# Kernel tuning notes

Measured on AMD Instinct MI355X. Metric: run time of the kernel, lower is better.

The kernel has to match this reference:

```python
import jax, jax.numpy as jnp
import numpy as np

HEADS = 8
NEG_SLOPE = 0.2


def _layer_norm(x, g, b, eps=1e-5):
    mu = x.mean(-1, keepdims=True)
    var = ((x - mu) ** 2).mean(-1, keepdims=True)
    return (x - mu) / jnp.sqrt(var + eps) * g + b


def setup_inputs() -> dict:
    key = jax.random.key(0)
    ks = jax.random.split(key, 24)
    N, E, H, L = 512, 260000, 256, 4
    s = 0.05
    return dict(
        x=jax.random.normal(ks[0], (N, 1), jnp.float32),
        edge_index=jax.random.randint(ks[1], (2, E), 0, N),
        edge_attr=jax.random.uniform(ks[2], (E, 3), jnp.float32),
        emb_W=jax.random.normal(ks[3], (1, H)) * s,
        emb_b=jnp.zeros((H,)),
        Wl=jax.random.normal(ks[4], (L, H, H)) * s,
        bl=jnp.zeros((L, H)),
        Wr=jax.random.normal(ks[5], (L, H, H)) * s,
        br=jnp.zeros((L, H)),
        We=jax.random.normal(ks[6], (L, 3, H)) * s,
        att=jax.random.normal(ks[7], (L, HEADS, H // HEADS)) * s,
        gb=jnp.zeros((L, H)),
        ln_g=jnp.ones((L, H)),
        ln_b=jnp.zeros((L, H)),
        p1_W=jax.random.normal(ks[8], (2 * H, H)) * s,
        p1_b=jnp.zeros((H,)),
        p2_W=jax.random.normal(ks[9], (H, H // 2)) * s,
        p2_b=jnp.zeros((H // 2,)),
        p3_W=jax.random.normal(ks[10], (H // 2, 1)) * s,
        p3_b=jnp.zeros((1,)),
        v1_W=jax.random.normal(ks[11], (2 * H, H)) * s,
        v1_b=jnp.zeros((H,)),
        v2_W=jax.random.normal(ks[12], (H, 1)) * s,
        v2_b=jnp.zeros((1,)),
        coupling=jnp.asarray(1.0, jnp.float32),
    )


def reference(x, edge_index, edge_attr, emb_W, emb_b, Wl, bl, Wr, br, We, att,
              gb, ln_g, ln_b, p1_W, p1_b, p2_W, p2_b, p3_W, p3_b,
              v1_W, v1_b, v2_W, v2_b, coupling):
    N = x.shape[0]
    E = edge_attr.shape[0]
    L = Wl.shape[0]
    C = Wl.shape[-1] // HEADS
    src, dst = edge_index[0], edge_index[1]

    # PyG GATv2Conv adds self-loops with edge_attr fill_value='mean'
    # (mean of incoming edge_attr per destination node).
    sums = jax.ops.segment_sum(edge_attr, dst, num_segments=N)
    cnt = jax.ops.segment_sum(jnp.ones((E,), edge_attr.dtype), dst, num_segments=N)
    self_attr = sums / jnp.maximum(cnt, 1.0)[:, None]
    loop = jnp.arange(N)
    src_f = jnp.concatenate([src, loop])            # [E+N]
    dst_f = jnp.concatenate([dst, loop])
    ea_f = jnp.concatenate([edge_attr, self_attr])  # [E+N, 3]

    h = x @ emb_W + emb_b                           # [N, H]
    for l in range(L):
        res = h
        xl = (h @ Wl[l] + bl[l]).reshape(N, HEADS, C)
        xr = (h @ Wr[l] + br[l]).reshape(N, HEADS, C)
        ee = (ea_f @ We[l]).reshape(-1, HEADS, C)
        # GATv2 scoring: leaky_relu(x_l[src]+x_r[dst]+edge) . att
        m = jax.nn.leaky_relu(xl[src_f] + xr[dst_f] + ee, NEG_SLOPE)
        alpha = jnp.einsum('ehc,hc->eh', m, att[l])
        amax = jax.ops.segment_max(alpha, dst_f, num_segments=N)
        alpha = jnp.exp(alpha - amax[dst_f])
        denom = jax.ops.segment_sum(alpha, dst_f, num_segments=N)
        alpha = alpha / denom[dst_f]
        out = jax.ops.segment_sum(xl[src_f] * alpha[..., None], dst_f,
                                  num_segments=N).reshape(N, HEADS * C) + gb[l]
        h = jax.nn.relu(_layer_norm(out + res, ln_g[l], ln_b[l]))

    # graph-level representation (single graph, batch=None branch)
    graph_repr = jnp.concatenate([h.mean(0, keepdims=True),
                                  h.max(0, keepdims=True)], axis=1)  # [1, 2H]

    # all-pairs edge representations (i < j)
    iu, ju = jnp.triu_indices(N, k=1)
    er = jnp.concatenate([h[iu], h[ju]], axis=1)    # [N(N-1)/2, 2H]
    p = jax.nn.relu(er @ p1_W + p1_b)
    p = jax.nn.relu(p @ p2_W + p2_b)
    policy_logits = (p @ p3_W + p3_b).squeeze(-1)   # [N(N-1)/2]

    v = jax.nn.relu(graph_repr @ v1_W + v1_b)
    value = (v @ v2_W + v2_b).squeeze(-1)           # [1]

    # Potts energy: per-color degree-squared approximation of triangles
    colors = jnp.argmax(edge_attr, axis=1)
    energy = jnp.asarray(0.0, h.dtype)
    for c in (1, 2):
        w = (colors == c).astype(h.dtype)
        deg = (jax.ops.segment_sum(w, src, num_segments=N)
               + jax.ops.segment_sum(w, dst, num_segments=N))
        energy = energy + (deg ** 2).sum() / (2.0 * N)
    energy = energy * coupling

    return policy_logits, value, energy
```

## Files before the change

### kernel.cpp

```cpp
#include <hip/hip_runtime.h>
#include <math.h>

#define HDIM 256
#define NHEADS 8
#define NEG 0.2f
#define NB 256
#define SEG 4

typedef float f32x4 __attribute__((ext_vector_type(4)));
typedef _Float16 f16x8 __attribute__((ext_vector_type(8)));
typedef __fp16 fp16v2 __attribute__((ext_vector_type(2)));

__global__ __launch_bounds__(256) void edge_part(
    const int* __restrict__ ei, const float* __restrict__ ea, int E, int CH,
    int* __restrict__ pcnt, float* __restrict__ psum, int* __restrict__ pcol) {
  __shared__ int   lcnt[512];
  __shared__ float ls0[512], ls1[512], ls2[512];
  __shared__ int   lcol[1024];
  int t = threadIdx.x, b = blockIdx.x;
  for (int n = t; n < 512; n += 256) {
    lcnt[n] = 0; ls0[n] = 0.f; ls1[n] = 0.f; ls2[n] = 0.f;
    lcol[n] = 0; lcol[512 + n] = 0;
  }
  __syncthreads();
  int e0 = b * CH, e1 = min(E, e0 + CH);
  for (int e = e0 + t; e < e1; e += 256) {
    int src = ei[e], dst = ei[E + e];
    float a0 = ea[3*e], a1 = ea[3*e+1], a2 = ea[3*e+2];
    atomicAdd(&lcnt[dst], 1);
    atomicAdd(&ls0[dst], a0);
    atomicAdd(&ls1[dst], a1);
    atomicAdd(&ls2[dst], a2);
    int idx = 0; float best = a0;
    if (a1 > best) { best = a1; idx = 1; }
    if (a2 > best) { idx = 2; }
    if (idx) {
      int o = (idx - 1) << 9;
      atomicAdd(&lcol[o + src], 1);
      atomicAdd(&lcol[o + dst], 1);
    }
  }
  __syncthreads();
  for (int n = t; n < 512; n += 256) {
    pcnt[b*512 + n] = lcnt[n];
    psum[(size_t)(0*NB + b)*512 + n] = ls0[n];
    psum[(size_t)(1*NB + b)*512 + n] = ls1[n];
    psum[(size_t)(2*NB + b)*512 + n] = ls2[n];
    pcol[(size_t)(0*NB + b)*512 + n] = lcol[n];
    pcol[(size_t)(1*NB + b)*512 + n] = lcol[512 + n];
  }
}

__global__ __launch_bounds__(256) void red_kernel(
    const int* __restrict__ pcnt, const float* __restrict__ psum,
    const int* __restrict__ pcol,
    int* __restrict__ cnt, float* __restrict__ sred, int* __restrict__ dred,
    int* __restrict__ pbase) {
  int q = blockIdx.x >> 1;
  int n = (blockIdx.x & 1)*256 + threadIdx.x;
  if (q == 0) {
    int run = 0;
#pragma unroll 8
    for (int b = 0; b < NB; ++b) {
      int v = pcnt[b*512 + n];
      pbase[b*512 + n] = run;
      run += v;
    }
    cnt[n] = run;
  } else if (q <= 3) {
    int qq = q - 1;
    float s = 0.f;
#pragma unroll 8
    for (int b = 0; b < NB; ++b) s += psum[(size_t)(qq*NB + b)*512 + n];
    sred[qq*512 + n] = s;
  } else {
    int qq = q - 4;
    int s = 0;
#pragma unroll 8
    for (int b = 0; b < NB; ++b) s += pcol[(size_t)(qq*NB + b)*512 + n];
    dred[qq*512 + n] = s;
  }
}

__global__ __launch_bounds__(512) void scan2(
    const int* __restrict__ cnt, const float* __restrict__ sred,
    const int* __restrict__ dred, int N,
    int* __restrict__ rowp, float4* __restrict__ csr,
    const float* __restrict__ coupling, float* __restrict__ eout) {
  int t = threadIdx.x;
  int c = (t < N) ? cnt[t] : 0;
  __shared__ int sbuf[512];
  int v = (t < N) ? (c + 1) : 0;
  sbuf[t] = v;
  __syncthreads();
  for (int off = 1; off < 512; off <<= 1) {
    int add = (t >= off) ? sbuf[t - off] : 0;
    __syncthreads();
    sbuf[t] += add;
    __syncthreads();
  }
  int incl = sbuf[t], excl = incl - v;
  if (t < N) {
    rowp[t] = excl;
    if (t == N - 1) rowp[N] = incl;
    float inv = 1.f / fmaxf((float)c, 1.f);
    csr[excl] = make_float4(sred[t]*inv, sred[512 + t]*inv, sred[1024 + t]*inv,
                            __int_as_float(t));
  }
  float e = 0.f;
  if (t < N) {
    float d1 = (float)dred[t], d2 = (float)dred[512 + t];
    e = d1*d1 + d2*d2;
  }
#pragma unroll
  for (int off = 1; off < 64; off <<= 1) e += __shfl_xor(e, off);
  __shared__ float wred[8];
  if ((t & 63) == 0) wred[t >> 6] = e;
  __syncthreads();
  if (t == 0) {
    float s = 0.f;
#pragma unroll
    for (int i = 0; i < 8; ++i) s += wred[i];
    eout[0] = coupling[0] * s / (2.f * (float)N);
  }
}

__global__ __launch_bounds__(256) void scatter2(
    const int* __restrict__ ei, const float* __restrict__ ea, int E, int CH,
    const int* __restrict__ rowp, const int* __restrict__ pbase,
    float4* __restrict__ csr) {
  __shared__ int lofs[512];
  int t = threadIdx.x, b = blockIdx.x;
  for (int n = t; n < 512; n += 256) lofs[n] = 0;
  __syncthreads();
  int e0 = b * CH, e1 = min(E, e0 + CH);
  for (int e = e0 + t; e < e1; e += 256) {
    int src = ei[e], dst = ei[E + e];
    float a0 = ea[3*e], a1 = ea[3*e+1], a2 = ea[3*e+2];
    int lp = atomicAdd(&lofs[dst], 1);
    int pos = rowp[dst] + 1 + pbase[b*512 + dst] + lp;
    csr[pos] = make_float4(a0, a1, a2, __int_as_float(src));
  }
}

__global__ __launch_bounds__(256) void emb_kernel(
    const float* __restrict__ x, const float* __restrict__ eW,
    const float* __restrict__ eb, float* __restrict__ h) {
  int n = blockIdx.x, t = threadIdx.x;
  h[n*HDIM + t] = fmaf(x[n], eW[t], eb[t]);
}

__global__ __launch_bounds__(256) void w_prep_all(
    const float* __restrict__ Wl, const float* __restrict__ Wr,
    const float* __restrict__ p1W, unsigned short* __restrict__ dst) {
  int gid = blockIdx.x * 256 + threadIdx.x;
  int s = gid >> 16, e = gid & 65535;
  int k = e >> 8, n = e & 255;
  const float* src = (s < 4) ? (Wl + (size_t)s*65536)
                   : (s < 8) ? (Wr + (size_t)(s-4)*65536)
                             : (p1W + (size_t)(s-8)*65536);
  int c = k >> 5, quad = (k >> 3) & 3, kj = k & 7;
  int nt = n >> 4, nl = n & 15;
  int lane = quad*16 + nl;
  _Float16 hv = (_Float16)src[(size_t)k*256 + n];
  dst[(size_t)s*65536 + ((nt*8 + c)*512 + lane*8 + kj)] = *(unsigned short*)&hv;
}

__global__ __launch_bounds__(256) void dual_gemm_mfma(
    const float* __restrict__ Hm,
    const unsigned short* __restrict__ W1h, const unsigned short* __restrict__ W2h,
    const float* __restrict__ b1, const float* __restrict__ b2,
    float* __restrict__ o1, float* __restrict__ o2,
    unsigned short* __restrict__ o1h) {
  int bx = blockIdx.x, by = blockIdx.y;
  int t = threadIdx.x, w = t >> 6, l = t & 63;
  int quad = l >> 4, nl = l & 15;
  int mt = bx*4 + w;

  const unsigned short* Wh; const float* bias; float* o; int nt;
  bool first = (by < 16);
  if (first) { Wh = W1h; bias = b1; o = o1; nt = by; }
  else       { Wh = W2h; bias = b2; o = o2; nt = by - 16; }

  const float* Ar = Hm + (size_t)(mt*16 + nl)*HDIM + quad*8;
  f32x4 acc = (f32x4){0.f, 0.f, 0.f, 0.f};

#pragma unroll
  for (int c = 0; c < 8; ++c) {
    float4 a0 = *(const float4*)(Ar + c*32);
    float4 a1 = *(const float4*)(Ar + c*32 + 4);
    union { f16x8 v8; fp16v2 v2[4]; } u;
    u.v2[0] = __builtin_amdgcn_cvt_pkrtz(a0.x, a0.y);
    u.v2[1] = __builtin_amdgcn_cvt_pkrtz(a0.z, a0.w);
    u.v2[2] = __builtin_amdgcn_cvt_pkrtz(a1.x, a1.y);
    u.v2[3] = __builtin_amdgcn_cvt_pkrtz(a1.z, a1.w);
    f16x8 bfrag = *(const f16x8*)(Wh + (size_t)((nt*8 + c)*512 + l*8));
    acc = __builtin_amdgcn_mfma_f32_16x16x32_f16(u.v8, bfrag, acc, 0, 0, 0);
  }

  int colg = nt*16 + nl;
  float bv = bias ? bias[colg] : 0.f;
#pragma unroll
  for (int r = 0; r < 4; ++r) {
    float val = acc[r] + bv;
    size_t idx = (size_t)(mt*16 + quad*4 + r)*HDIM + colg;
    o[idx] = val;
    if (first && o1h) {
      _Float16 hv = (_Float16)val;
      o1h[idx] = *(unsigned short*)&hv;
    }
  }
}

__global__ __launch_bounds__(256) void attn_gather(
    const unsigned short* __restrict__ xlh, const float* __restrict__ xr,
    const float4* __restrict__ csr, const int* __restrict__ row_start,
    const float* __restrict__ We, const float* __restrict__ att,
    float* __restrict__ pm, float* __restrict__ pl, float* __restrict__ pacc) {
  int nb = blockIdx.x;
  int n = nb >> 2, sgm = nb & (SEG - 1);
  int t = threadIdx.x;
  int g = t >> 5, l = t & 31, hd = l >> 2, qd = l & 3;
  int cb = hd*32 + qd*8;

  float xrv[8], w0[8], w1[8], w2[8], av[8];
#pragma unroll
  for (int j = 0; j < 8; ++j) {
    xrv[j] = xr[(size_t)n*HDIM + cb + j];
    w0[j]  = We[cb + j];
    w1[j]  = We[HDIM + cb + j];
    w2[j]  = We[2*HDIM + cb + j];
    av[j]  = att[cb + j];
  }
  int rs = row_start[n], re = row_start[n+1], len = re - rs;
  int s0 = rs + ((len * sgm) >> 2);
  int s1 = rs + ((len * (sgm + 1)) >> 2);

  float mh = -INFINITY, lh = 0.f;
  float acc[8] = {0.f,0.f,0.f,0.f,0.f,0.f,0.f,0.f};

  int idx = s0 + g;
  if (idx < s1) {
    float4 rec = csr[idx];
    while (idx < s1) {
      int idxn = idx + 8;
      float4 recn = csr[idxn < s1 ? idxn : rs];
      int s = __float_as_int(rec.w);
      union { f16x8 v8; _Float16 h[8]; } ux;
      ux.v8 = *(const f16x8*)(xlh + (size_t)s*HDIM + cb);
      float xv[8];
#pragma unroll
      for (int j = 0; j < 8; ++j) xv[j] = (float)ux.h[j];
      float partial = 0.f;
#pragma unroll
      for (int j = 0; j < 8; ++j) {
        float m = fmaf(rec.z, w2[j], fmaf(rec.y, w1[j], fmaf(rec.x, w0[j], xrv[j]))) + xv[j];
        m = fmaxf(m, NEG * m);
        partial = fmaf(m, av[j], partial);
      }
      partial += __shfl_xor(partial, 1);
      partial += __shfl_xor(partial, 2);
      if (partial > mh) {
        float sc = __expf(mh - partial);
        lh *= sc;
#pragma unroll
        for (int j = 0; j < 8; ++j) acc[j] *= sc;
        mh = partial;
      }
      float pw = __expf(partial - mh);
      lh += pw;
#pragma unroll
      for (int j = 0; j < 8; ++j) acc[j] = fmaf(pw, xv[j], acc[j]);
      rec = recn; idx = idxn;
    }
  }

  __shared__ float lacc[8][HDIM];
  __shared__ float lm[8][NHEADS];
  __shared__ float llv[8][NHEADS];
#pragma unroll
  for (int j = 0; j < 8; ++j) lacc[g][cb + j] = acc[j];
  if (qd == 0) { lm[g][hd] = mh; llv[g][hd] = lh; }
  __syncthreads();

  int c = t, hh = c >> 5;
  float M = -INFINITY;
#pragma unroll
  for (int g2 = 0; g2 < 8; ++g2) M = fmaxf(M, lm[g2][hh]);
  float L = 0.f, o = 0.f;
#pragma unroll
  for (int g2 = 0; g2 < 8; ++g2) {
    float e2 = __expf(lm[g2][hh] - M);
    L = fmaf(llv[g2][hh], e2, L);
    o = fmaf(lacc[g2][c], e2, o);
  }
  pacc[(size_t)nb*HDIM + c] = o;
  if ((c & 31) == 0) {
    pm[nb*NHEADS + hh] = M;
    pl[nb*NHEADS + hh] = L;
  }
}

__global__ __launch_bounds__(256) void attn_merge(
    const float* __restrict__ pm, const float* __restrict__ pl,
    const float* __restrict__ pacc,
    const float* __restrict__ gb, const float* __restrict__ lng,
    const float* __restrict__ lnb,
    const float* __restrict__ h_in, float* __restrict__ h_out) {
  int n = blockIdx.x, t = threadIdx.x;
  int c = t, hh = c >> 5;
  float M = -INFINITY;
#pragma unroll
  for (int s = 0; s < SEG; ++s) M = fmaxf(M, pm[(n*SEG + s)*NHEADS + hh]);
  float L = 0.f, o = 0.f;
#pragma unroll
  for (int s = 0; s < SEG; ++s) {
    float e2 = __expf(pm[(n*SEG + s)*NHEADS + hh] - M);
    L = fmaf(pl[(n*SEG + s)*NHEADS + hh], e2, L);
    o = fmaf(pacc[(size_t)(n*SEG + s)*HDIM + c], e2, o);
  }
  float val = o / L + gb[c] + h_in[(size_t)n*HDIM + c];

  float s1 = val, s2 = val * val;
#pragma unroll
  for (int off = 1; off < 64; off <<= 1) {
    s1 += __shfl_xor(s1, off);
    s2 += __shfl_xor(s2, off);
  }
  __shared__ float rs1[4], rs2[4];
  if ((t & 63) == 0) { rs1[t >> 6] = s1; rs2[t >> 6] = s2; }
  __syncthreads();
  float S1 = rs1[0] + rs1[1] + rs1[2] + rs1[3];
  float S2 = rs2[0] + rs2[1] + rs2[2] + rs2[3];
  float mu = S1 * (1.f/HDIM);
  float var = S2 * (1.f/HDIM) - mu * mu;
  float y = (val - mu) * rsqrtf(var + 1e-5f);
  y = fmaf(y, lng[c], lnb[c]);
  h_out[(size_t)n*HDIM + c] = fmaxf(y, 0.f);
}

__global__ __launch_bounds__(256) void w2_prep_kernel(
    const float* __restrict__ W2, unsigned short* __restrict__ W2h) {
  int tid = blockIdx.x * 256 + threadIdx.x;
  int k = tid >> 7, n = tid & 127;
  int c = k >> 5, kq = (k >> 3) & 3, kj = k & 7;
  int nt = n >> 4, nl = n & 15;
  int lane = kq*16 + nl;
  _Float16 hv = (_Float16)W2[(size_t)k*128 + n];
  W2h[(size_t)(((c*8 + nt)*64 + lane)*8 + kj)] = *(unsigned short*)&hv;
}

__global__ __launch_bounds__(256, 4) void pair_mfma_kernel(
    const float* __restrict__ A, const float* __restrict__ Bm,
    const unsigned short* __restrict__ W2h,
    const float* __restrict__ b2, const float* __restrict__ W3,
    const float* __restrict__ b3, float* __restrict__ out, int N) {
  int bb = blockIdx.x;
  int half = bb & 1;
  int b = bb >> 1, ti = 0, rem = 32;
  while (b >= rem) { b -= rem; ti++; rem--; }
  int tj = ti + b;
  int i0 = ti * 16 + half * 8;
  int j0 = tj * 16;

  int t = threadIdx.x;
  int w = t >> 6, l = t & 63;
  int quad = l >> 4, nl = l & 15;

  float b2v[8], w3v[8];
#pragma unroll
  for (int nt = 0; nt < 8; ++nt) {
    b2v[nt] = b2[nt*16 + nl];
    w3v[nt] = W3[nt*16 + nl];
  }

  const float* Brow = Bm + (size_t)(j0 + nl) * HDIM;
  const float* Arow0 = A + (size_t)(i0 + w*2) * HDIM;

  f32x4 acc[2][8];
#pragma unroll
  for (int a2 = 0; a2 < 2; ++a2)
#pragma unroll
    for (int nt = 0; nt < 8; ++nt) acc[a2][nt] = (f32x4){0.f,0.f,0.f,0.f};

  for (int c = 0; c < 8; ++c) {
    int kb = c*32 + quad*8;
    float4 bv0 = *(const float4*)(Brow + kb);
    float4 bv1 = *(const float4*)(Brow + kb + 4);

    f16x8 afrag[2];
#pragma unroll
    for (int a2 = 0; a2 < 2; ++a2) {
      const float* Ar = Arow0 + (size_t)a2*HDIM + kb;
      float4 av0 = *(const float4*)Ar;
      float4 av1 = *(const float4*)(Ar + 4);
      union { f16x8 v8; fp16v2 v2[4]; } u;
      u.v2[0] = __builtin_amdgcn_cvt_pkrtz(fmaxf(av0.x + bv0.x, 0.f),
                                           fmaxf(av0.y + bv0.y, 0.f));
      u.v2[1] = __builtin_amdgcn_cvt_pkrtz(fmaxf(av0.z + bv0.z, 0.f),
                                           fmaxf(av0.w + bv0.w, 0.f));
      u.v2[2] = __builtin_amdgcn_cvt_pkrtz(fmaxf(av1.x + bv1.x, 0.f),
                                           fmaxf(av1.y + bv1.y, 0.f));
      u.v2[3] = __builtin_amdgcn_cvt_pkrtz(fmaxf(av1.z + bv1.z, 0.f),
                                           fmaxf(av1.w + bv1.w, 0.f));
      afrag[a2] = u.v8;
    }

#pragma unroll
    for (int nt = 0; nt < 8; ++nt) {
      f16x8 bfrag = *(const f16x8*)(W2h + (size_t)(((c*8 + nt)*64 + l) * 8));
#pragma unroll
      for (int a2 = 0; a2 < 2; ++a2)
        acc[a2][nt] = __builtin_amdgcn_mfma_f32_16x16x32_f16(
            afrag[a2], bfrag, acc[a2][nt], 0, 0, 0);
    }
  }

  float b3v = b3[0];
#pragma unroll
  for (int a2 = 0; a2 < 2; ++a2) {
    int i = i0 + w*2 + a2;
#pragma unroll
    for (int r = 0; r < 4; ++r) {
      float s = 0.f;
#pragma unroll
      for (int nt = 0; nt < 8; ++nt)
        s = fmaf(fmaxf(acc[a2][nt][r] + b2v[nt], 0.f), w3v[nt], s);
      s += __shfl_xor(s, 1);
      s += __shfl_xor(s, 2);
      s += __shfl_xor(s, 4);
      s += __shfl_xor(s, 8);
      if (nl == 0) {
        int j = j0 + quad*4 + r;
        if (i < j)
          out[(size_t)i*(2*N - i - 1)/2 + (j - i - 1)] = s + b3v;
      }
    }
  }
}

__global__ __launch_bounds__(256) void pool_kernel(
    const float* __restrict__ h, float* __restrict__ psums,
    float* __restrict__ pmaxs) {
  int g = blockIdx.x, t = threadIdx.x;
  float s = 0.f, m = -INFINITY;
#pragma unroll
  for (int r = 0; r < 16; ++r) {
    float v = h[(size_t)(g*16 + r)*HDIM + t];
    s += v; m = fmaxf(m, v);
  }
  psums[g*HDIM + t] = s;
  pmaxs[g*HDIM + t] = m;
}

__global__ __launch_bounds__(256) void value1_kernel(
    const float* __restrict__ psums, const float* __restrict__ pmaxs,
    const float* __restrict__ v1W, float* __restrict__ vpart, int N) {
  int b = blockIdx.x, t = threadIdx.x;
  int k0 = b * 16;
  int kk = t >> 4, g = t & 15;
  __shared__ float repr16[16];
  int k = k0 + kk;
  float v;
  if (k < HDIM) {
    v = psums[g*HDIM + k] + psums[(g + 16)*HDIM + k];
    v += __shfl_xor(v, 1); v += __shfl_xor(v, 2);
    v += __shfl_xor(v, 4); v += __shfl_xor(v, 8);
    if (g == 0) repr16[kk] = v / (float)N;
  } else {
    int kc = k - HDIM;
    v = fmaxf(pmaxs[g*HDIM + kc], pmaxs[(g + 16)*HDIM + kc]);
    v = fmaxf(v, __shfl_xor(v, 1)); v = fmaxf(v, __shfl_xor(v, 2));
    v = fmaxf(v, __shfl_xor(v, 4)); v = fmaxf(v, __shfl_xor(v, 8));
    if (g == 0) repr16[kk] = v;
  }
  __syncthreads();
  float pv = 0.f;
#pragma unroll
  for (int q = 0; q < 16; ++q)
    pv = fmaf(repr16[q], v1W[(size_t)(k0 + q)*HDIM + t], pv);
  vpart[b*HDIM + t] = pv;
}

__global__ __launch_bounds__(256) void value2_kernel(
    const float* __restrict__ vpart, const float* __restrict__ v1b,
    const float* __restrict__ v2W, const float* __restrict__ v2b,
    float* __restrict__ out) {
  int t = threadIdx.x;
  float a = 0.f;
#pragma unroll
  for (int g = 0; g < 32; ++g) a += vpart[g*HDIM + t];
  a = fmaxf(a + v1b[t], 0.f);
  float pv = a * v2W[t];
#pragma unroll
  for (int off = 1; off < 64; off <<= 1) pv += __shfl_xor(pv, off);
  __shared__ float wsum[4];
  if ((t & 63) == 0) wsum[t >> 6] = pv;
  __syncthreads();
  if (t == 0) out[0] = wsum[0] + wsum[1] + wsum[2] + wsum[3] + v2b[0];
}

extern "C" void kernel_launch(void* const* d_in, const int* in_sizes, int n_in,
                              void* d_out, int out_size, void* d_ws, size_t ws_size,
                              hipStream_t stream) {
  const float* x    = (const float*)d_in[0];
  const int*   ei   = (const int*)  d_in[1];
  const float* ea   = (const float*)d_in[2];
  const float* embW = (const float*)d_in[3];
  const float* embb = (const float*)d_in[4];
  const float* Wl   = (const float*)d_in[5];
  const float* bl   = (const float*)d_in[6];
  const float* Wr   = (const float*)d_in[7];
  const float* br   = (const float*)d_in[8];
  const float* We   = (const float*)d_in[9];
  const float* att  = (const float*)d_in[10];
  const float* gb   = (const float*)d_in[11];
  const float* lng  = (const float*)d_in[12];
  const float* lnb  = (const float*)d_in[13];
  const float* p1W  = (const float*)d_in[14];
  const float* p1b  = (const float*)d_in[15];
  const float* p2W  = (const float*)d_in[16];
  const float* p2b  = (const float*)d_in[17];
  const float* p3W  = (const float*)d_in[18];
  const float* p3b  = (const float*)d_in[19];
  const float* v1W  = (const float*)d_in[20];
  const float* v1b  = (const float*)d_in[21];
  const float* v2W  = (const float*)d_in[22];
  const float* v2b  = (const float*)d_in[23];
  const float* coup = (const float*)d_in[24];

  int N = in_sizes[0];
  int E = in_sizes[2] / 3;
  float* out = (float*)d_out;
  size_t P = (size_t)N*(N-1)/2;

  char* w = (char*)d_ws;
  int*    rowp = (int*)   (w + 0);
  float*  plS  = (float*) (w + 2560);
  float*  plM  = (float*) (w + 35328);
  float*  vprt = (float*) (w + 68096);
  float4* csr  = (float4*)(w + 101120);
  size_t csr_end = 101120 + (size_t)(E + N) * 16;
  csr_end = (csr_end + 255) & ~(size_t)255;
  float* hA  = (float*)(w + csr_end);
  float* hB  = hA  + (size_t)N*HDIM;
  float* xlb = hB  + (size_t)N*HDIM;
  float* xrb = xlb + (size_t)N*HDIM;
  float* Ab  = xrb + (size_t)N*HDIM;
  float* Bb  = Ab  + (size_t)N*HDIM;
  unsigned short* xlh   = (unsigned short*)(Bb + (size_t)N*HDIM);
  unsigned short* W2h   = xlh + (size_t)N*HDIM;
  unsigned short* Whall = W2h + 32768;
  size_t ubase = ((size_t)((char*)(Whall + 10*65536) - w) + 255) & ~(size_t)255;

  char* U = w + ubase;
  int*    pcnt = (int*)   (U + 0);
  float*  psum = (float*) (U + 524288);
  int*    pcol = (int*)   (U + 2097152);
  int*    pbase= (int*)   (U + 3145728);
  int*    cnt  = (int*)   (U + 3670016);
  float*  sred = (float*) (U + 3672064);
  int*    dred = (int*)   (U + 3678208);
  float*  pmv  = (float*) (U + 0);
  float*  plv  = (float*) (U + 65536);
  float*  pacc = (float*) (U + 131072);

  int CH = (E + NB - 1) / NB;
  edge_part<<<NB, 256, 0, stream>>>(ei, ea, E, CH, pcnt, psum, pcol);
  red_kernel<<<12, 256, 0, stream>>>(pcnt, psum, pcol, cnt, sred, dred, pbase);
  scan2<<<1, 512, 0, stream>>>(cnt, sred, dred, N, rowp, csr, coup, out + P + 1);
  scatter2<<<NB, 256, 0, stream>>>(ei, ea, E, CH, rowp, pbase, csr);
  emb_kernel<<<N, 256, 0, stream>>>(x, embW, embb, hA);
  w2_prep_kernel<<<128, 256, 0, stream>>>(p2W, W2h);
  w_prep_all<<<2560, 256, 0, stream>>>(Wl, Wr, p1W, Whall);

  float* hin = hA;
  float* hout = hB;
  for (int l = 0; l < 4; ++l) {
    dual_gemm_mfma<<<dim3(8, 32), 256, 0, stream>>>(hin,
        Whall + (size_t)l*65536, Whall + (size_t)(4 + l)*65536,
        bl + l*HDIM, br + l*HDIM, xlb, xrb, xlh);
    attn_gather<<<N*SEG, 256, 0, stream>>>(xlh, xrb, csr, rowp,
        We + (size_t)l*3*HDIM, att + (size_t)l*HDIM, pmv, plv, pacc);
    attn_merge<<<N, 256, 0, stream>>>(pmv, plv, pacc,
        gb + (size_t)l*HDIM, lng + (size_t)l*HDIM, lnb + (size_t)l*HDIM,
        hin, hout);
    float* tmp = hin; hin = hout; hout = tmp;
  }

  dual_gemm_mfma<<<dim3(8, 32), 256, 0, stream>>>(hin,
      Whall + (size_t)8*65536, Whall + (size_t)9*65536,
      p1b, (const float*)nullptr, Ab, Bb, (unsigned short*)nullptr);

  pair_mfma_kernel<<<1056, 256, 0, stream>>>(Ab, Bb, W2h, p2b, p3W, p3b, out, N);

  pool_kernel<<<32, 256, 0, stream>>>(hin, plS, plM);
  value1_kernel<<<32, 256, 0, stream>>>(plS, plM, v1W, vprt, N);
  value2_kernel<<<1, 256, 0, stream>>>(vprt, v1b, v2W, v2b, out + P);
}
```

Baseline: 315.1 us.

## Fuse attention merge, embedding, weight prep and value head via last-block reductions

Removes several small kernel launches. The embedding is computed inside the first GEMM and the first merge, and the p2 weight prep joins the main weight-prep kernel. The attention merge and layernorm now run in whichever of the four segment blocks per node finishes last, detected with an atomic counter. The pool, value1 and value2 kernels become one kernel that uses the same last-block scheme. This trades launch overhead for atomics, fences and counters that must be zeroed on every call.

Result: slower. 1.239 ms (+293.2%).

```diff
diff --git a/kernel.cpp b/kernel.cpp
--- a/kernel.cpp
+++ b/kernel.cpp
@@ -10,6 +10,8 @@
 typedef float f32x4 __attribute__((ext_vector_type(4)));
 typedef _Float16 f16x8 __attribute__((ext_vector_type(8)));
 typedef __fp16 fp16v2 __attribute__((ext_vector_type(2)));
+
+#define AGENT __HIP_MEMORY_SCOPE_AGENT
 
 __global__ __launch_bounds__(256) void edge_part(
     const int* __restrict__ ei, const float* __restrict__ ea, int E, int CH,
@@ -143,31 +145,41 @@
   }
 }
 
-__global__ __launch_bounds__(256) void emb_kernel(
-    const float* __restrict__ x, const float* __restrict__ eW,
-    const float* __restrict__ eb, float* __restrict__ h) {
-  int n = blockIdx.x, t = threadIdx.x;
-  h[n*HDIM + t] = fmaf(x[n], eW[t], eb[t]);
-}
-
 __global__ __launch_bounds__(256) void w_prep_all(
     const float* __restrict__ Wl, const float* __restrict__ Wr,
-    const float* __restrict__ p1W, unsigned short* __restrict__ dst) {
+    const float* __restrict__ p1W, const float* __restrict__ W2,
+    unsigned short* __restrict__ dst, unsigned short* __restrict__ W2h,
+    int* __restrict__ ctr, int* __restrict__ vctr) {
   int gid = blockIdx.x * 256 + threadIdx.x;
-  int s = gid >> 16, e = gid & 65535;
-  int k = e >> 8, n = e & 255;
-  const float* src = (s < 4) ? (Wl + (size_t)s*65536)
-                   : (s < 8) ? (Wr + (size_t)(s-4)*65536)
-                             : (p1W + (size_t)(s-8)*65536);
-  int c = k >> 5, quad = (k >> 3) & 3, kj = k & 7;
-  int nt = n >> 4, nl = n & 15;
-  int lane = quad*16 + nl;
-  _Float16 hv = (_Float16)src[(size_t)k*256 + n];
-  dst[(size_t)s*65536 + ((nt*8 + c)*512 + lane*8 + kj)] = *(unsigned short*)&hv;
+  if (gid < 4*512 + 1) {
+    if (gid < 4*512) ctr[gid] = 0; else vctr[0] = 0;
+  }
+  if (gid < 10*65536) {
+    int s = gid >> 16, e = gid & 65535;
+    int k = e >> 8, n = e & 255;
+    const float* src = (s < 4) ? (Wl + (size_t)s*65536)
+                     : (s < 8) ? (Wr + (size_t)(s-4)*65536)
+                               : (p1W + (size_t)(s-8)*65536);
+    int c = k >> 5, quad = (k >> 3) & 3, kj = k & 7;
+    int nt = n >> 4, nl = n & 15;
+    int lane = quad*16 + nl;
+    _Float16 hv = (_Float16)src[(size_t)k*256 + n];
+    dst[(size_t)s*65536 + ((nt*8 + c)*512 + lane*8 + kj)] = *(unsigned short*)&hv;
+  } else {
+    int e = gid - 10*65536;
+    int k = e >> 7, n = e & 127;
+    int c = k >> 5, kq = (k >> 3) & 3, kj = k & 7;
+    int nt = n >> 4, nl = n & 15;
+    int lane = kq*16 + nl;
+    _Float16 hv = (_Float16)W2[(size_t)k*128 + n];
+    W2h[(size_t)(((c*8 + nt)*64 + lane)*8 + kj)] = *(unsigned short*)&hv;
+  }
 }
 
 __global__ __launch_bounds__(256) void dual_gemm_mfma(
     const float* __restrict__ Hm,
+    const float* __restrict__ x, const float* __restrict__ embW,
+    const float* __restrict__ embb,
     const unsigned short* __restrict__ W1h, const unsigned short* __restrict__ W2h,
     const float* __restrict__ b1, const float* __restrict__ b2,
     float* __restrict__ o1, float* __restrict__ o2,
@@ -182,13 +194,28 @@
   if (first) { Wh = W1h; bias = b1; o = o1; nt = by; }
   else       { Wh = W2h; bias = b2; o = o2; nt = by - 16; }
 
-  const float* Ar = Hm + (size_t)(mt*16 + nl)*HDIM + quad*8;
+  int row = mt*16 + nl;
+  const float* Ar = Hm ? (Hm + (size_t)row*HDIM + quad*8) : nullptr;
+  float xm = Hm ? 0.f : x[row];
   f32x4 acc = (f32x4){0.f, 0.f, 0.f, 0.f};
 
 #pragma unroll
   for (int c = 0; c < 8; ++c) {
-    float4 a0 = *(const float4*)(Ar + c*32);
-    float4 a1 = *(const float4*)(Ar + c*32 + 4);
+    float4 a0, a1;
+    if (Hm) {
+      a0 = *(const float4*)(Ar + c*32);
+      a1 = *(const float4*)(Ar + c*32 + 4);
+    } else {
+      int kb = c*32 + quad*8;
+      float4 e0 = *(const float4*)(embW + kb);
+      float4 e1 = *(const float4*)(embW + kb + 4);
+      float4 c0 = *(const float4*)(embb + kb);
+      float4 c1 = *(const float4*)(embb + kb + 4);
+      a0 = make_float4(fmaf(xm, e0.x, c0.x), fmaf(xm, e0.y, c0.y),
+                       fmaf(xm, e0.z, c0.z), fmaf(xm, e0.w, c0.w));
+      a1 = make_float4(fmaf(xm, e1.x, c1.x), fmaf(xm, e1.y, c1.y),
+                       fmaf(xm, e1.z, c1.z), fmaf(xm, e1.w, c1.w));
+    }
     union { f16x8 v8; fp16v2 v2[4]; } u;
     u.v2[0] = __builtin_amdgcn_cvt_pkrtz(a0.x, a0.y);
     u.v2[1] = __builtin_amdgcn_cvt_pkrtz(a0.z, a0.w);
@@ -212,11 +239,18 @@
   }
 }
 
-__global__ __launch_bounds__(256) void attn_gather(
+__global__ __launch_bounds__(256) void attn_fused(
     const unsigned short* __restrict__ xlh, const float* __restrict__ xr,
     const float4* __restrict__ csr, const int* __restrict__ row_start,
     const float* __restrict__ We, const float* __restrict__ att,
-    float* __restrict__ pm, float* __restrict__ pl, float* __restrict__ pacc) {
+    float* __restrict__ pm, float* __restrict__ pl, float* __restrict__ pacc,
+    int* __restrict__ ctr,
+    const float* __restrict__ gb, const float* __restrict__ lng,
+    const float* __restrict__ lnb,
+    const float* __restrict__ h_in,
+    const float* __restrict__ x, const float* __restrict__ embW,
+    const float* __restrict__ embb,
+    float* __restrict__ h_out) {
   int nb = blockIdx.x;
   int n = nb >> 2, sgm = nb & (SEG - 1);
   int t = threadIdx.x;
@@ -294,41 +328,48 @@
     L = fmaf(llv[g2][hh], e2, L);
     o = fmaf(lacc[g2][c], e2, o);
   }
-  pacc[(size_t)nb*HDIM + c] = o;
+  __hip_atomic_store(&pacc[(size_t)nb*HDIM + c], o, __ATOMIC_RELAXED, AGENT);
   if ((c & 31) == 0) {
-    pm[nb*NHEADS + hh] = M;
-    pl[nb*NHEADS + hh] = L;
-  }
-}
-
-__global__ __launch_bounds__(256) void attn_merge(
-    const float* __restrict__ pm, const float* __restrict__ pl,
-    const float* __restrict__ pacc,
-    const float* __restrict__ gb, const float* __restrict__ lng,
-    const float* __restrict__ lnb,
-    const float* __restrict__ h_in, float* __restrict__ h_out) {
-  int n = blockIdx.x, t = threadIdx.x;
-  int c = t, hh = c >> 5;
-  float M = -INFINITY;
-#pragma unroll
-  for (int s = 0; s < SEG; ++s) M = fmaxf(M, pm[(n*SEG + s)*NHEADS + hh]);
-  float L = 0.f, o = 0.f;
+    __hip_atomic_store(&pm[nb*NHEADS + hh], M, __ATOMIC_RELAXED, AGENT);
+    __hip_atomic_store(&pl[nb*NHEADS + hh], L, __ATOMIC_RELAXED, AGENT);
+  }
+  __threadfence();
+  __syncthreads();
+  __shared__ int lastf;
+  if (t == 0) {
+    int old = __hip_atomic_fetch_add(&ctr[n], 1, __ATOMIC_ACQ_REL, AGENT);
+    lastf = (old == SEG - 1);
+  }
+  __syncthreads();
+  if (!lastf) return;
+  __threadfence();
+
+  float M2 = -INFINITY, ms[SEG];
 #pragma unroll
   for (int s = 0; s < SEG; ++s) {
-    float e2 = __expf(pm[(n*SEG + s)*NHEADS + hh] - M);
-    L = fmaf(pl[(n*SEG + s)*NHEADS + hh], e2, L);
-    o = fmaf(pacc[(size_t)(n*SEG + s)*HDIM + c], e2, o);
-  }
-  float val = o / L + gb[c] + h_in[(size_t)n*HDIM + c];
-
-  float s1 = val, s2 = val * val;
+    ms[s] = __hip_atomic_load(&pm[(n*SEG + s)*NHEADS + hh], __ATOMIC_RELAXED, AGENT);
+    M2 = fmaxf(M2, ms[s]);
+  }
+  float L2 = 0.f, o2 = 0.f;
+#pragma unroll
+  for (int s = 0; s < SEG; ++s) {
+    float e2 = __expf(ms[s] - M2);
+    float ls = __hip_atomic_load(&pl[(n*SEG + s)*NHEADS + hh], __ATOMIC_RELAXED, AGENT);
+    float os = __hip_atomic_load(&pacc[(size_t)(n*SEG + s)*HDIM + c], __ATOMIC_RELAXED, AGENT);
+    L2 = fmaf(ls, e2, L2);
+    o2 = fmaf(os, e2, o2);
+  }
+  float hi = h_in ? h_in[(size_t)n*HDIM + c] : fmaf(x[n], embW[c], embb[c]);
+  float val = o2 / L2 + gb[c] + hi;
+
+  float s1v = val, s2v = val * val;
 #pragma unroll
   for (int off = 1; off < 64; off <<= 1) {
-    s1 += __shfl_xor(s1, off);
-    s2 += __shfl_xor(s2, off);
+    s1v += __shfl_xor(s1v, off);
+    s2v += __shfl_xor(s2v, off);
   }
   __shared__ float rs1[4], rs2[4];
-  if ((t & 63) == 0) { rs1[t >> 6] = s1; rs2[t >> 6] = s2; }
+  if ((t & 63) == 0) { rs1[t >> 6] = s1v; rs2[t >> 6] = s2v; }
   __syncthreads();
   float S1 = rs1[0] + rs1[1] + rs1[2] + rs1[3];
   float S2 = rs2[0] + rs2[1] + rs2[2] + rs2[3];
@@ -337,17 +378,6 @@
   float y = (val - mu) * rsqrtf(var + 1e-5f);
   y = fmaf(y, lng[c], lnb[c]);
   h_out[(size_t)n*HDIM + c] = fmaxf(y, 0.f);
-}
-
-__global__ __launch_bounds__(256) void w2_prep_kernel(
-    const float* __restrict__ W2, unsigned short* __restrict__ W2h) {
-  int tid = blockIdx.x * 256 + threadIdx.x;
-  int k = tid >> 7, n = tid & 127;
-  int c = k >> 5, kq = (k >> 3) & 3, kj = k & 7;
-  int nt = n >> 4, nl = n & 15;
-  int lane = kq*16 + nl;
-  _Float16 hv = (_Float16)W2[(size_t)k*128 + n];
-  W2h[(size_t)(((c*8 + nt)*64 + lane)*8 + kj)] = *(unsigned short*)&hv;
 }
 
 __global__ __launch_bounds__(256, 4) void pair_mfma_kernel(
@@ -439,23 +469,11 @@
   }
 }
 
-__global__ __launch_bounds__(256) void pool_kernel(
-    const float* __restrict__ h, float* __restrict__ psums,
-    float* __restrict__ pmaxs) {
-  int g = blockIdx.x, t = threadIdx.x;
-  float s = 0.f, m = -INFINITY;
-#pragma unroll
-  for (int r = 0; r < 16; ++r) {
-    float v = h[(size_t)(g*16 + r)*HDIM + t];
-    s += v; m = fmaxf(m, v);
-  }
-  psums[g*HDIM + t] = s;
-  pmaxs[g*HDIM + t] = m;
-}
-
-__global__ __launch_bounds__(256) void value1_kernel(
-    const float* __restrict__ psums, const float* __restrict__ pmaxs,
-    const float* __restrict__ v1W, float* __restrict__ vpart, int N) {
+__global__ __launch_bounds__(256) void value_fused(
+    const float* __restrict__ h, const float* __restrict__ v1W,
+    const float* __restrict__ v1b, const float* __restrict__ v2W,
+    const float* __restrict__ v2b, float* __restrict__ vpart,
+    int* __restrict__ vctr, float* __restrict__ out, int N) {
   int b = blockIdx.x, t = threadIdx.x;
   int k0 = b * 16;
   int kk = t >> 4, g = t & 15;
@@ -463,13 +481,15 @@
   int k = k0 + kk;
   float v;
   if (k < HDIM) {
-    v = psums[g*HDIM + k] + psums[(g + 16)*HDIM + k];
+    v = 0.f;
+    for (int r = g; r < N; r += 16) v += h[(size_t)r*HDIM + k];
     v += __shfl_xor(v, 1); v += __shfl_xor(v, 2);
     v += __shfl_xor(v, 4); v += __shfl_xor(v, 8);
     if (g == 0) repr16[kk] = v / (float)N;
   } else {
     int kc = k - HDIM;
-    v = fmaxf(pmaxs[g*HDIM + kc], pmaxs[(g + 16)*HDIM + kc]);
+    v = -INFINITY;
+    for (int r = g; r < N; r += 16) v = fmaxf(v, h[(size_t)r*HDIM + kc]);
     v = fmaxf(v, __shfl_xor(v, 1)); v = fmaxf(v, __shfl_xor(v, 2));
     v = fmaxf(v, __shfl_xor(v, 4)); v = fmaxf(v, __shfl_xor(v, 8));
     if (g == 0) repr16[kk] = v;
@@ -479,23 +499,27 @@
 #pragma unroll
   for (int q = 0; q < 16; ++q)
     pv = fmaf(repr16[q], v1W[(size_t)(k0 + q)*HDIM + t], pv);
-  vpart[b*HDIM + t] = pv;
-}
-
-__global__ __launch_bounds__(256) void value2_kernel(
-    const float* __restrict__ vpart, const float* __restrict__ v1b,
-    const float* __restrict__ v2W, const float* __restrict__ v2b,
-    float* __restrict__ out) {
-  int t = threadIdx.x;
+  __hip_atomic_store(&vpart[b*HDIM + t], pv, __ATOMIC_RELAXED, AGENT);
+  __threadfence();
+  __syncthreads();
+  __shared__ int lastf;
+  if (t == 0) {
+    int old = __hip_atomic_fetch_add(vctr, 1, __ATOMIC_ACQ_REL, AGENT);
+    lastf = (old == 31);
+  }
+  __syncthreads();
+  if (!lastf) return;
+  __threadfence();
   float a = 0.f;
 #pragma unroll
-  for (int g = 0; g < 32; ++g) a += vpart[g*HDIM + t];
+  for (int gg = 0; gg < 32; ++gg)
+    a += __hip_atomic_load(&vpart[gg*HDIM + t], __ATOMIC_RELAXED, AGENT);
   a = fmaxf(a + v1b[t], 0.f);
-  float pv = a * v2W[t];
-#pragma unroll
-  for (int off = 1; off < 64; off <<= 1) pv += __shfl_xor(pv, off);
+  float fv = a * v2W[t];
+#pragma unroll
+  for (int off = 1; off < 64; off <<= 1) fv += __shfl_xor(fv, off);
   __shared__ float wsum[4];
-  if ((t & 63) == 0) wsum[t >> 6] = pv;
+  if ((t & 63) == 0) wsum[t >> 6] = fv;
   __syncthreads();
   if (t == 0) out[0] = wsum[0] + wsum[1] + wsum[2] + wsum[3] + v2b[0];
 }
@@ -536,11 +560,11 @@
 
   char* w = (char*)d_ws;
   int*    rowp = (int*)   (w + 0);
-  float*  plS  = (float*) (w + 2560);
-  float*  plM  = (float*) (w + 35328);
-  float*  vprt = (float*) (w + 68096);
-  float4* csr  = (float4*)(w + 101120);
-  size_t csr_end = 101120 + (size_t)(E + N) * 16;
+  float*  vprt = (float*) (w + 2560);
+  int*    ctr  = (int*)   (w + 35328);
+  int*    vctr = (int*)   (w + 43520);
+  float4* csr  = (float4*)(w + 43776);
+  size_t csr_end = 43776 + (size_t)(E + N) * 16;
   csr_end = (csr_end + 255) & ~(size_t)255;
   float* hA  = (float*)(w + csr_end);
   float* hB  = hA  + (size_t)N*HDIM;
@@ -570,31 +594,29 @@
   red_kernel<<<12, 256, 0, stream>>>(pcnt, psum, pcol, cnt, sred, dred, pbase);
   scan2<<<1, 512, 0, stream>>>(cnt, sred, dred, N, rowp, csr, coup, out + P + 1);
   scatter2<<<NB, 256, 0, stream>>>(ei, ea, E, CH, rowp, pbase, csr);
-  emb_kernel<<<N, 256, 0, stream>>>(x, embW, embb, hA);
-  w2_prep_kernel<<<128, 256, 0, stream>>>(p2W, W2h);
-  w_prep_all<<<2560, 256, 0, stream>>>(Wl, Wr, p1W, Whall);
-
-  float* hin = hA;
+  w_prep_all<<<2688, 256, 0, stream>>>(Wl, Wr, p1W, p2W, Whall, W2h, ctr, vctr);
+
+  float* hin = nullptr;
   float* hout = hB;
   for (int l = 0; l < 4; ++l) {
-    dual_gemm_mfma<<<dim3(8, 32), 256, 0, stream>>>(hin,
+    dual_gemm_mfma<<<dim3(8, 32), 256, 0, stream>>>(hin, x, embW, embb,
         Whall + (size_t)l*65536, Whall + (size_t)(4 + l)*65536,
         bl + l*HDIM, br + l*HDIM, xlb, xrb, xlh);
-    attn_gather<<<N*SEG, 256, 0, stream>>>(xlh, xrb, csr, rowp,
-        We + (size_t)l*3*HDIM, att + (size_t)l*HDIM, pmv, plv, pacc);
-    attn_merge<<<N, 256, 0, stream>>>(pmv, plv, pacc,
+    attn_fused<<<N*SEG, 256, 0, stream>>>(xlh, xrb, csr, rowp,
+        We + (size_t)l*3*HDIM, att + (size_t)l*HDIM, pmv, plv, pacc,
+        ctr + l*512,
         gb + (size_t)l*HDIM, lng + (size_t)l*HDIM, lnb + (size_t)l*HDIM,
-        hin, hout);
-    float* tmp = hin; hin = hout; hout = tmp;
-  }
-
-  dual_gemm_mfma<<<dim3(8, 32), 256, 0, stream>>>(hin,
+        hin, x, embW, embb, hout);
+    hin = hout;
+    hout = (hout == hB) ? hA : hB;
+  }
+
+  dual_gemm_mfma<<<dim3(8, 32), 256, 0, stream>>>(hin, x, embW, embb,
       Whall + (size_t)8*65536, Whall + (size_t)9*65536,
       p1b, (const float*)nullptr, Ab, Bb, (unsigned short*)nullptr);
 
   pair_mfma_kernel<<<1056, 256, 0, stream>>>(Ab, Bb, W2h, p2b, p3W, p3b, out, N);
 
-  pool_kernel<<<32, 256, 0, stream>>>(hin, plS, plM);
-  value1_kernel<<<32, 256, 0, stream>>>(plS, plM, v1W, vprt, N);
-  value2_kernel<<<1, 256, 0, stream>>>(vprt, v1b, v2W, v2b, out + P);
-}
+  value_fused<<<32, 256, 0, stream>>>(hin, v1W, v1b, v2W, v2b,
+                                      vprt, vctr, out + P, N);
+}
```

## Fuse attention gather and merge into one 1024-thread block per node; fold embedding

Applied to the files above, without the earlier changes.

Replaces the four-segment attention gather plus separate merge/LayerNorm kernel with a single kernel that uses 32 edge groups per destination node and performs the softmax merge, residual, LayerNorm and ReLU in-block. The embedding kernel is removed by computing the embedding on the fly in the first GEMM and the first attention residual, and the W2 prep is merged into the weight-prep kernel. This removes several launches and the partial-result round trips through global memory. In exchange it uses larger blocks with more shared memory, which may reduce occupancy and leave load imbalance across nodes.

Result: slower. 322.4 us (+2.3%).

```diff
diff --git a/kernel.cpp b/kernel.cpp
--- a/kernel.cpp
+++ b/kernel.cpp
@@ -5,7 +5,7 @@
 #define NHEADS 8
 #define NEG 0.2f
 #define NB 256
-#define SEG 4
+#define NG 32
 
 typedef float f32x4 __attribute__((ext_vector_type(4)));
 typedef _Float16 f16x8 __attribute__((ext_vector_type(8)));
@@ -143,31 +143,37 @@
   }
 }
 
-__global__ __launch_bounds__(256) void emb_kernel(
-    const float* __restrict__ x, const float* __restrict__ eW,
-    const float* __restrict__ eb, float* __restrict__ h) {
-  int n = blockIdx.x, t = threadIdx.x;
-  h[n*HDIM + t] = fmaf(x[n], eW[t], eb[t]);
-}
-
 __global__ __launch_bounds__(256) void w_prep_all(
     const float* __restrict__ Wl, const float* __restrict__ Wr,
-    const float* __restrict__ p1W, unsigned short* __restrict__ dst) {
+    const float* __restrict__ p1W, const float* __restrict__ W2,
+    unsigned short* __restrict__ dst, unsigned short* __restrict__ W2h) {
   int gid = blockIdx.x * 256 + threadIdx.x;
-  int s = gid >> 16, e = gid & 65535;
-  int k = e >> 8, n = e & 255;
-  const float* src = (s < 4) ? (Wl + (size_t)s*65536)
-                   : (s < 8) ? (Wr + (size_t)(s-4)*65536)
-                             : (p1W + (size_t)(s-8)*65536);
-  int c = k >> 5, quad = (k >> 3) & 3, kj = k & 7;
-  int nt = n >> 4, nl = n & 15;
-  int lane = quad*16 + nl;
-  _Float16 hv = (_Float16)src[(size_t)k*256 + n];
-  dst[(size_t)s*65536 + ((nt*8 + c)*512 + lane*8 + kj)] = *(unsigned short*)&hv;
+  if (gid < 10*65536) {
+    int s = gid >> 16, e = gid & 65535;
+    int k = e >> 8, n = e & 255;
+    const float* src = (s < 4) ? (Wl + (size_t)s*65536)
+                     : (s < 8) ? (Wr + (size_t)(s-4)*65536)
+                               : (p1W + (size_t)(s-8)*65536);
+    int c = k >> 5, quad = (k >> 3) & 3, kj = k & 7;
+    int nt = n >> 4, nl = n & 15;
+    int lane = quad*16 + nl;
+    _Float16 hv = (_Float16)src[(size_t)k*256 + n];
+    dst[(size_t)s*65536 + ((nt*8 + c)*512 + lane*8 + kj)] = *(unsigned short*)&hv;
+  } else {
+    int e = gid - 10*65536;
+    int k = e >> 7, n = e & 127;
+    int c = k >> 5, kq = (k >> 3) & 3, kj = k & 7;
+    int nt = n >> 4, nl = n & 15;
+    int lane = kq*16 + nl;
+    _Float16 hv = (_Float16)W2[(size_t)k*128 + n];
+    W2h[(size_t)(((c*8 + nt)*64 + lane)*8 + kj)] = *(unsigned short*)&hv;
+  }
 }
 
 __global__ __launch_bounds__(256) void dual_gemm_mfma(
     const float* __restrict__ Hm,
+    const float* __restrict__ x, const float* __restrict__ embW,
+    const float* __restrict__ embb,
     const unsigned short* __restrict__ W1h, const unsigned short* __restrict__ W2h,
     const float* __restrict__ b1, const float* __restrict__ b2,
     float* __restrict__ o1, float* __restrict__ o2,
@@ -182,13 +188,28 @@
   if (first) { Wh = W1h; bias = b1; o = o1; nt = by; }
   else       { Wh = W2h; bias = b2; o = o2; nt = by - 16; }
 
-  const float* Ar = Hm + (size_t)(mt*16 + nl)*HDIM + quad*8;
+  int row = mt*16 + nl;
+  const float* Ar = Hm ? (Hm + (size_t)row*HDIM + quad*8) : nullptr;
+  float xm = Hm ? 0.f : x[row];
   f32x4 acc = (f32x4){0.f, 0.f, 0.f, 0.f};
 
 #pragma unroll
   for (int c = 0; c < 8; ++c) {
-    float4 a0 = *(const float4*)(Ar + c*32);
-    float4 a1 = *(const float4*)(Ar + c*32 + 4);
+    float4 a0, a1;
+    if (Hm) {
+      a0 = *(const float4*)(Ar + c*32);
+      a1 = *(const float4*)(Ar + c*32 + 4);
+    } else {
+      int kb = c*32 + quad*8;
+      float4 e0 = *(const float4*)(embW + kb);
+      float4 e1 = *(const float4*)(embW + kb + 4);
+      float4 c0 = *(const float4*)(embb + kb);
+      float4 c1 = *(const float4*)(embb + kb + 4);
+      a0 = make_float4(fmaf(xm, e0.x, c0.x), fmaf(xm, e0.y, c0.y),
+                       fmaf(xm, e0.z, c0.z), fmaf(xm, e0.w, c0.w));
+      a1 = make_float4(fmaf(xm, e1.x, c1.x), fmaf(xm, e1.y, c1.y),
+                       fmaf(xm, e1.z, c1.z), fmaf(xm, e1.w, c1.w));
+    }
     union { f16x8 v8; fp16v2 v2[4]; } u;
     u.v2[0] = __builtin_amdgcn_cvt_pkrtz(a0.x, a0.y);
     u.v2[1] = __builtin_amdgcn_cvt_pkrtz(a0.z, a0.w);
@@ -212,13 +233,17 @@
   }
 }
 
-__global__ __launch_bounds__(256) void attn_gather(
+__global__ __launch_bounds__(1024) void attn_one(
     const unsigned short* __restrict__ xlh, const float* __restrict__ xr,
-    const float4* __restrict__ csr, const int* __restrict__ row_start,
+    const float4* __restrict__ csr, const int* __restrict__ rowp,
     const float* __restrict__ We, const float* __restrict__ att,
-    float* __restrict__ pm, float* __restrict__ pl, float* __restrict__ pacc) {
-  int nb = blockIdx.x;
-  int n = nb >> 2, sgm = nb & (SEG - 1);
+    const float* __restrict__ gb, const float* __restrict__ lng,
+    const float* __restrict__ lnb,
+    const float* __restrict__ h_in,
+    const float* __restrict__ x, const float* __restrict__ embW,
+    const float* __restrict__ embb,
+    float* __restrict__ h_out) {
+  int n = blockIdx.x;
   int t = threadIdx.x;
   int g = t >> 5, l = t & 31, hd = l >> 2, qd = l & 3;
   int cb = hd*32 + qd*8;
@@ -232,19 +257,17 @@
     w2[j]  = We[2*HDIM + cb + j];
     av[j]  = att[cb + j];
   }
-  int rs = row_start[n], re = row_start[n+1], len = re - rs;
-  int s0 = rs + ((len * sgm) >> 2);
-  int s1 = rs + ((len * (sgm + 1)) >> 2);
+  int rs = rowp[n], re = rowp[n+1];
 
   float mh = -INFINITY, lh = 0.f;
   float acc[8] = {0.f,0.f,0.f,0.f,0.f,0.f,0.f,0.f};
 
-  int idx = s0 + g;
-  if (idx < s1) {
+  int idx = rs + g;
+  if (idx < re) {
     float4 rec = csr[idx];
-    while (idx < s1) {
-      int idxn = idx + 8;
-      float4 recn = csr[idxn < s1 ? idxn : rs];
+    while (idx < re) {
+      int idxn = idx + NG;
+      float4 recn = csr[idxn < re ? idxn : rs];
       int s = __float_as_int(rec.w);
       union { f16x8 v8; _Float16 h[8]; } ux;
       ux.v8 = *(const f16x8*)(xlh + (size_t)s*HDIM + cb);
@@ -275,79 +298,48 @@
     }
   }
 
-  __shared__ float lacc[8][HDIM];
-  __shared__ float lm[8][NHEADS];
-  __shared__ float llv[8][NHEADS];
+  __shared__ float lacc[NG][HDIM];
+  __shared__ float lm[NG][NHEADS];
+  __shared__ float llv[NG][NHEADS];
 #pragma unroll
   for (int j = 0; j < 8; ++j) lacc[g][cb + j] = acc[j];
   if (qd == 0) { lm[g][hd] = mh; llv[g][hd] = lh; }
   __syncthreads();
 
-  int c = t, hh = c >> 5;
-  float M = -INFINITY;
-#pragma unroll
-  for (int g2 = 0; g2 < 8; ++g2) M = fmaxf(M, lm[g2][hh]);
-  float L = 0.f, o = 0.f;
-#pragma unroll
-  for (int g2 = 0; g2 < 8; ++g2) {
-    float e2 = __expf(lm[g2][hh] - M);
-    L = fmaf(llv[g2][hh], e2, L);
-    o = fmaf(lacc[g2][c], e2, o);
-  }
-  pacc[(size_t)nb*HDIM + c] = o;
-  if ((c & 31) == 0) {
-    pm[nb*NHEADS + hh] = M;
-    pl[nb*NHEADS + hh] = L;
-  }
-}
-
-__global__ __launch_bounds__(256) void attn_merge(
-    const float* __restrict__ pm, const float* __restrict__ pl,
-    const float* __restrict__ pacc,
-    const float* __restrict__ gb, const float* __restrict__ lng,
-    const float* __restrict__ lnb,
-    const float* __restrict__ h_in, float* __restrict__ h_out) {
-  int n = blockIdx.x, t = threadIdx.x;
-  int c = t, hh = c >> 5;
-  float M = -INFINITY;
-#pragma unroll
-  for (int s = 0; s < SEG; ++s) M = fmaxf(M, pm[(n*SEG + s)*NHEADS + hh]);
-  float L = 0.f, o = 0.f;
-#pragma unroll
-  for (int s = 0; s < SEG; ++s) {
-    float e2 = __expf(pm[(n*SEG + s)*NHEADS + hh] - M);
-    L = fmaf(pl[(n*SEG + s)*NHEADS + hh], e2, L);
-    o = fmaf(pacc[(size_t)(n*SEG + s)*HDIM + c], e2, o);
-  }
-  float val = o / L + gb[c] + h_in[(size_t)n*HDIM + c];
-
-  float s1 = val, s2 = val * val;
-#pragma unroll
-  for (int off = 1; off < 64; off <<= 1) {
-    s1 += __shfl_xor(s1, off);
-    s2 += __shfl_xor(s2, off);
-  }
-  __shared__ float rs1[4], rs2[4];
-  if ((t & 63) == 0) { rs1[t >> 6] = s1; rs2[t >> 6] = s2; }
-  __syncthreads();
-  float S1 = rs1[0] + rs1[1] + rs1[2] + rs1[3];
-  float S2 = rs2[0] + rs2[1] + rs2[2] + rs2[3];
-  float mu = S1 * (1.f/HDIM);
-  float var = S2 * (1.f/HDIM) - mu * mu;
-  float y = (val - mu) * rsqrtf(var + 1e-5f);
-  y = fmaf(y, lng[c], lnb[c]);
-  h_out[(size_t)n*HDIM + c] = fmaxf(y, 0.f);
-}
-
-__global__ __launch_bounds__(256) void w2_prep_kernel(
-    const float* __restrict__ W2, unsigned short* __restrict__ W2h) {
-  int tid = blockIdx.x * 256 + threadIdx.x;
-  int k = tid >> 7, n = tid & 127;
-  int c = k >> 5, kq = (k >> 3) & 3, kj = k & 7;
-  int nt = n >> 4, nl = n & 15;
-  int lane = kq*16 + nl;
-  _Float16 hv = (_Float16)W2[(size_t)k*128 + n];
-  W2h[(size_t)(((c*8 + nt)*64 + lane)*8 + kj)] = *(unsigned short*)&hv;
+  __shared__ float rsum1[4], rsum2[4];
+  float val = 0.f;
+  if (t < HDIM) {
+    int c = t, hh = c >> 5;
+    float M = -INFINITY;
+#pragma unroll
+    for (int g2 = 0; g2 < NG; ++g2) M = fmaxf(M, lm[g2][hh]);
+    float L = 0.f, o = 0.f;
+#pragma unroll
+    for (int g2 = 0; g2 < NG; ++g2) {
+      float e2 = __expf(lm[g2][hh] - M);
+      L = fmaf(llv[g2][hh], e2, L);
+      o = fmaf(lacc[g2][c], e2, o);
+    }
+    float hi = h_in ? h_in[(size_t)n*HDIM + c] : fmaf(x[n], embW[c], embb[c]);
+    val = o / L + gb[c] + hi;
+    float s1v = val, s2v = val * val;
+#pragma unroll
+    for (int off = 1; off < 64; off <<= 1) {
+      s1v += __shfl_xor(s1v, off);
+      s2v += __shfl_xor(s2v, off);
+    }
+    if ((t & 63) == 0) { rsum1[t >> 6] = s1v; rsum2[t >> 6] = s2v; }
+  }
+  __syncthreads();
+  if (t < HDIM) {
+    float S1 = rsum1[0] + rsum1[1] + rsum1[2] + rsum1[3];
+    float S2 = rsum2[0] + rsum2[1] + rsum2[2] + rsum2[3];
+    float mu = S1 * (1.f/HDIM);
+    float var = S2 * (1.f/HDIM) - mu * mu;
+    float y = (val - mu) * rsqrtf(var + 1e-5f);
+    y = fmaf(y, lng[t], lnb[t]);
+    h_out[(size_t)n*HDIM + t] = fmaxf(y, 0.f);
+  }
 }
 
 __global__ __launch_bounds__(256, 4) void pair_mfma_kernel(
@@ -561,34 +553,29 @@
   int*    cnt  = (int*)   (U + 3670016);
   float*  sred = (float*) (U + 3672064);
   int*    dred = (int*)   (U + 3678208);
-  float*  pmv  = (float*) (U + 0);
-  float*  plv  = (float*) (U + 65536);
-  float*  pacc = (float*) (U + 131072);
 
   int CH = (E + NB - 1) / NB;
   edge_part<<<NB, 256, 0, stream>>>(ei, ea, E, CH, pcnt, psum, pcol);
   red_kernel<<<12, 256, 0, stream>>>(pcnt, psum, pcol, cnt, sred, dred, pbase);
   scan2<<<1, 512, 0, stream>>>(cnt, sred, dred, N, rowp, csr, coup, out + P + 1);
   scatter2<<<NB, 256, 0, stream>>>(ei, ea, E, CH, rowp, pbase, csr);
-  emb_kernel<<<N, 256, 0, stream>>>(x, embW, embb, hA);
-  w2_prep_kernel<<<128, 256, 0, stream>>>(p2W, W2h);
-  w_prep_all<<<2560, 256, 0, stream>>>(Wl, Wr, p1W, Whall);
-
-  float* hin = hA;
+  w_prep_all<<<2688, 256, 0, stream>>>(Wl, Wr, p1W, p2W, Whall, W2h);
+
+  float* hin = nullptr;
   float* hout = hB;
   for (int l = 0; l < 4; ++l) {
-    dual_gemm_mfma<<<dim3(8, 32), 256, 0, stream>>>(hin,
+    dual_gemm_mfma<<<dim3(8, 32), 256, 0, stream>>>(hin, x, embW, embb,
         Whall + (size_t)l*65536, Whall + (size_t)(4 + l)*65536,
         bl + l*HDIM, br + l*HDIM, xlb, xrb, xlh);
-    attn_gather<<<N*SEG, 256, 0, stream>>>(xlh, xrb, csr, rowp,
-        We + (size_t)l*3*HDIM, att + (size_t)l*HDIM, pmv, plv, pacc);
-    attn_merge<<<N, 256, 0, stream>>>(pmv, plv, pacc,
+    attn_one<<<N, 1024, 0, stream>>>(xlh, xrb, csr, rowp,
+        We + (size_t)l*3*HDIM, att + (size_t)l*HDIM,
         gb + (size_t)l*HDIM, lng + (size_t)l*HDIM, lnb + (size_t)l*HDIM,
-        hin, hout);
-    float* tmp = hin; hin = hout; hout = tmp;
-  }
-
-  dual_gemm_mfma<<<dim3(8, 32), 256, 0, stream>>>(hin,
+        hin, x, embW, embb, hout);
+    hin = hout;
+    hout = (hout == hB) ? hA : hB;
+  }
+
+  dual_gemm_mfma<<<dim3(8, 32), 256, 0, stream>>>(hin, x, embW, embb,
       Whall + (size_t)8*65536, Whall + (size_t)9*65536,
       p1b, (const float*)nullptr, Ab, Bb, (unsigned short*)nullptr);
 
```
